# Optimization experiments

Hardware: AMD Instinct MI355X
Metric: run time of the kernel (lower is better)

## Reference

```python
import jax, jax.numpy as jnp
import numpy as np

# Model dims (from ModelArgs defaults)
B, S, DIM = 1, 1024, 2880
H, HKV, HD = 64, 8, 64        # query heads, kv heads, head dim
GROUP = H // HKV              # 8 query heads per kv head
WINDOW = 128                  # sliding window (layer_idx=0 -> active)
THETA = 150000.0


def setup_inputs() -> dict:
    key = jax.random.key(0)
    ks = jax.random.split(key, 10)
    rn = lambda k, shape, sc: (jax.random.normal(k, shape, jnp.float32) * sc)
    return {
        "x": rn(ks[0], (B, S, DIM), 1.0),
        "wq_w": rn(ks[1], (H * HD, DIM), 0.02),
        "wq_b": rn(ks[2], (H * HD,), 0.02),
        "wk_w": rn(ks[3], (HKV * HD, DIM), 0.02),
        "wk_b": rn(ks[4], (HKV * HD,), 0.02),
        "wv_w": rn(ks[5], (HKV * HD, DIM), 0.02),
        "wv_b": rn(ks[6], (HKV * HD,), 0.02),
        "wo_w": rn(ks[7], (DIM, H * HD), 0.02),
        "wo_b": rn(ks[8], (DIM,), 0.02),
        "sinks": rn(ks[9], (H,), 1.0),
    }


def _rope(t):
    # t: [B, S, h, HD]; half-split (rotate_half) RoPE with base THETA
    half = HD // 2
    inv_freq = 1.0 / (THETA ** (jnp.arange(half, dtype=jnp.float32) * 2.0 / HD))
    ang = jnp.arange(S, dtype=jnp.float32)[:, None] * inv_freq      # [S, half]
    cos = jnp.cos(ang)[None, :, None, :]
    sin = jnp.sin(ang)[None, :, None, :]
    t1, t2 = t[..., :half], t[..., half:]
    return jnp.concatenate([t1 * cos - t2 * sin, t1 * sin + t2 * cos], axis=-1)


def reference(x, wq_w, wq_b, wk_w, wk_b, wv_w, wv_b, wo_w, wo_b, sinks):
    # Projections (nn.Linear: y = x @ W^T + b)
    q = (jnp.einsum('bsd,ed->bse', x, wq_w) + wq_b).reshape(B, S, H, HD)
    k = (jnp.einsum('bsd,ed->bse', x, wk_w) + wk_b).reshape(B, S, HKV, HD)
    v = (jnp.einsum('bsd,ed->bse', x, wv_w) + wv_b).reshape(B, S, HKV, HD)

    q = _rope(q)
    k = _rope(k)

    # GQA: expand kv heads to match query heads
    k = jnp.repeat(k, GROUP, axis=2)   # [B, S, H, HD]
    v = jnp.repeat(v, GROUP, axis=2)

    scale = HD ** -0.5
    scores = jnp.einsum('bihd,bjhd->bhij', q, k) * scale   # [B, H, S, S]

    # Causal + sliding-window mask: attend to j with 0 <= i-j < WINDOW
    i = jnp.arange(S)[:, None]
    j = jnp.arange(S)[None, :]
    allowed = (j <= i) & ((i - j) < WINDOW)
    scores = jnp.where(allowed, scores, jnp.float32(-1e30))

    # Softmax with per-head learnable sink logit folded into normalization
    sink = sinks[None, :, None, None]                       # [1, H, 1, 1]
    m = jnp.maximum(jnp.max(scores, axis=-1, keepdims=True), sink)
    e = jnp.exp(scores - m)
    denom = jnp.sum(e, axis=-1, keepdims=True) + jnp.exp(sink - m)
    probs = e / denom                                       # sink mass dropped

    out = jnp.einsum('bhij,bjhd->bihd', probs, v).reshape(B, S, H * HD)
    return jnp.einsum('bse,de->bsd', out, wo_w) + wo_b
```

## Files before the change

kernel.cpp:

```cpp
#include <hip/hip_runtime.h>

typedef __attribute__((ext_vector_type(4))) float f32x4;
typedef __attribute__((ext_vector_type(8))) short s16x8;
typedef unsigned short u16;

#define DEVI __device__ __forceinline__

DEVI u16 f2bf(float f) {
    union { float f; unsigned int u; } v; v.f = f;
    unsigned int r = v.u + 0x7FFFu + ((v.u >> 16) & 1u);
    return (u16)(r >> 16);
}
DEVI float bf2f(u16 b) {
    union { unsigned int u; float f; } v; v.u = ((unsigned int)b) << 16;
    return v.f;
}

typedef __attribute__((address_space(1))) void gv_t;
typedef __attribute__((address_space(3))) void sv_t;

#define GLOAD16(SRC, DST) __builtin_amdgcn_global_load_lds( \
    (gv_t*)(SRC), (sv_t*)(DST), 16, 0, 0)

DEVI f32x4 mfma_bf16(s16x8 a, s16x8 b, f32x4 c) {
    return __builtin_amdgcn_mfma_f32_16x16x32_bf16(a, b, c, 0, 0, 0);
}

__global__ void cvt1_kernel(
    const float* __restrict__ x,  const float* __restrict__ wq, const float* __restrict__ wk,
    const float* __restrict__ wv,
    u16* __restrict__ xb, u16* __restrict__ wqb, u16* __restrict__ wkb,
    u16* __restrict__ wvb)
{
    int id = blockIdx.x * 256 + threadIdx.x;
    const float* s; u16* d; int off;
    if      (id < 737280)  { s = x;  d = xb;  off = id; }
    else if (id < 3686400) { s = wq; d = wqb; off = id - 737280; }
    else if (id < 4055040) { s = wk; d = wkb; off = id - 3686400; }
    else                   { s = wv; d = wvb; off = id - 4055040; }
    f32x4 v = *(const f32x4*)(s + (size_t)off * 4);
    union { u16 u[4]; unsigned long long ll; } o;
    #pragma unroll
    for (int j = 0; j < 4; ++j) o.u[j] = f2bf(v[j]);
    *(unsigned long long*)(d + (size_t)off * 4) = o.ll;
}

__global__ void cvt_wo_kernel(const float* __restrict__ wo, u16* __restrict__ wob)
{
    int id = blockIdx.x * 256 + threadIdx.x;
    f32x4 v = *(const f32x4*)(wo + (size_t)id * 4);
    union { u16 u[4]; unsigned long long ll; } o;
    #pragma unroll
    for (int j = 0; j < 4; ++j) o.u[j] = f2bf(v[j]);
    *(unsigned long long*)(wob + (size_t)id * 4) = o.ll;
}

__global__ __launch_bounds__(256, 2) void gemm_bf16nt(
    const u16* __restrict__ A, int lda, int kit, int ntot,
    const u16* __restrict__ W0, int t0, int n0, int c0,
    const u16* __restrict__ W1, int t1, int n1, int c1,
    const u16* __restrict__ W2, int t2, int n2, int c2,
    u16* __restrict__ C, int ldc, long long cstride)
{
    __shared__ u16 Als[2][128 * 64];
    __shared__ u16 Bls[2][128 * 64];

    const int lin = blockIdx.x;
    const int xc  = lin & 7;
    const int mm  = lin >> 3;
    const int nbl = xc + 8 * (mm >> 3);
    const int yt  = mm & 7;
    if (nbl >= ntot) return;

    const int tid  = threadIdx.x;
    const int lane = tid & 63;
    const int wid  = tid >> 6;
    const int li   = lane & 15;
    const int lg   = lane >> 4;
    const int m0   = yt * 128;

    const u16* W; int nt0, nsz, cb;
    if (nbl < t0)           { W = W0; nt0 = nbl * 128;             nsz = n0; cb = c0; }
    else if (nbl < t0 + t1) { W = W1; nt0 = (nbl - t0) * 128;      nsz = n1; cb = c1; }
    else                    { W = W2; nt0 = (nbl - t0 - t1) * 128; nsz = n2; cb = c2; }

    const int z  = blockIdx.z;
    const int S  = gridDim.z;
    const int it0 = (z * kit) / S;
    const int it1 = ((z + 1) * kit) / S;
    u16* Cp = C + (long long)z * cstride;

    const int wm = (wid >> 1) * 64;
    const int wn = (wid & 1) * 64;

    f32x4 acc[4][4];
    #pragma unroll
    for (int mi = 0; mi < 4; ++mi)
        #pragma unroll
        for (int ni = 0; ni < 4; ++ni)
            acc[mi][ni] = (f32x4){0.f, 0.f, 0.f, 0.f};

    const int srow = tid >> 3;
    const int slc  = (tid & 7) ^ (srow & 7);

#define STAGE(BUF, IT)                                                          \
    do {                                                                        \
        int k0_ = (IT) * 64;                                                    \
        _Pragma("unroll")                                                       \
        for (int s_ = 0; s_ < 4; ++s_) {                                        \
            const u16* sa_ = A + (size_t)(m0 + s_ * 32 + srow) * lda + k0_ + slc * 8; \
            GLOAD16(sa_, &Als[BUF][(s_ * 256 + wid * 64) * 8]);                 \
        }                                                                       \
        _Pragma("unroll")                                                       \
        for (int s_ = 0; s_ < 4; ++s_) {                                        \
            int wr_ = nt0 + s_ * 32 + srow;                                     \
            if (wr_ > nsz - 1) wr_ = nsz - 1;                                   \
            const u16* sb_ = W + (size_t)wr_ * lda + k0_ + slc * 8;             \
            GLOAD16(sb_, &Bls[BUF][(s_ * 256 + wid * 64) * 8]);                 \
        }                                                                       \
    } while (0)

    STAGE(0, it0);
    asm volatile("" ::: "memory");
    STAGE(1, it0 + 1);

    for (int it = it0; it < it1; ++it) {
        const int cur = (it - it0) & 1;

        if (it + 1 < it1) {
            asm volatile("s_waitcnt vmcnt(8)\n\ts_barrier" ::: "memory");
        } else {
            asm volatile("s_waitcnt vmcnt(0)\n\ts_barrier" ::: "memory");
        }

        s16x8 af[4][2], bfv[4][2];
        #pragma unroll
        for (int mi = 0; mi < 4; ++mi)
            #pragma unroll
            for (int kc = 0; kc < 2; ++kc) {
                int row = wm + mi * 16 + li;
                int ch  = (kc * 4 + lg) ^ (row & 7);
                af[mi][kc] = *(const s16x8*)&Als[cur][row * 64 + ch * 8];
            }
        #pragma unroll
        for (int ni = 0; ni < 4; ++ni)
            #pragma unroll
            for (int kc = 0; kc < 2; ++kc) {
                int row = wn + ni * 16 + li;
                int ch  = (kc * 4 + lg) ^ (row & 7);
                bfv[ni][kc] = *(const s16x8*)&Bls[cur][row * 64 + ch * 8];
            }
        #pragma unroll
        for (int mi = 0; mi < 4; ++mi)
            #pragma unroll
            for (int ni = 0; ni < 4; ++ni)
                #pragma unroll
                for (int kc = 0; kc < 2; ++kc)
                    acc[mi][ni] = mfma_bf16(af[mi][kc], bfv[ni][kc], acc[mi][ni]);

        asm volatile("s_waitcnt lgkmcnt(0)\n\ts_barrier" ::: "memory");

        if (it + 2 < it1) STAGE(cur, it + 2);
    }
#undef STAGE

    #pragma unroll
    for (int ni = 0; ni < 4; ++ni) {
        int colr = nt0 + wn + ni * 16 + li;
        if (colr < nsz) {
            #pragma unroll
            for (int mi = 0; mi < 4; ++mi)
                #pragma unroll
                for (int r = 0; r < 4; ++r) {
                    int row = m0 + wm + mi * 16 + lg * 4 + r;
                    Cp[(size_t)row * ldc + cb + colr] = f2bf(acc[mi][ni][r]);
                }
        }
    }
}

__global__ void rope_kernel(const u16* __restrict__ qkvp,
                            const float* __restrict__ qb, const float* __restrict__ kb,
                            const float* __restrict__ vb,
                            u16* __restrict__ qo, u16* __restrict__ ko, u16* __restrict__ vo)
{
    const long long PST = 1024LL * 5120;
    int id = blockIdx.x * 256 + threadIdx.x;
    int s  = id / 2560;
    int r  = id % 2560;
    const u16* r0 = qkvp + (size_t)s * 5120;
    if (r < 2304) {
        bool isq = r < 2048;
        int rr   = isq ? r : r - 2048;
        int hh   = rr >> 5;
        int d    = rr & 31;
        int col  = (isq ? 0 : 4096) + hh * 64 + d;
        int bcol = isq ? col : col - 4096;
        const float* bias = isq ? qb : kb;
        float t1 = bf2f(r0[col])      + bf2f(r0[col + PST])      + bf2f(r0[col + 2 * PST])      + bias[bcol];
        float t2 = bf2f(r0[col + 32]) + bf2f(r0[col + 32 + PST]) + bf2f(r0[col + 32 + 2 * PST]) + bias[bcol + 32];
        float ang = (float)s * exp2f((float)d * -0.5373314f);
        float sn, cs;
        sincosf(ang, &sn, &cs);
        float sc = isq ? 0.125f : 1.0f;
        float o1 = (t1 * cs - t2 * sn) * sc;
        float o2 = (t1 * sn + t2 * cs) * sc;
        u16* dst = isq ? qo : ko;
        int ldd  = isq ? 4096 : 512;
        dst[(size_t)s * ldd + bcol]      = f2bf(o1);
        dst[(size_t)s * ldd + bcol + 32] = f2bf(o2);
    } else {
        int e = (r - 2304) * 2;
        int c0 = 4608 + e;
        float v0 = bf2f(r0[c0])     + bf2f(r0[c0 + PST])     + bf2f(r0[c0 + 2 * PST])     + vb[e];
        float v1 = bf2f(r0[c0 + 1]) + bf2f(r0[c0 + 1 + PST]) + bf2f(r0[c0 + 1 + 2 * PST]) + vb[e + 1];
        vo[(size_t)s * 512 + e]     = f2bf(v0);
        vo[(size_t)s * 512 + e + 1] = f2bf(v1);
    }
}

__global__ void reduce_out_kernel(const u16* __restrict__ parts,
                                  const float* __restrict__ bias,
                                  float* __restrict__ out)
{
    int id = blockIdx.x * 256 + threadIdx.x;
    const long long stride = 1024LL * 2880;
    long long base = (long long)id * 8;
    float s[8];
    #pragma unroll
    for (int j = 0; j < 8; ++j) s[j] = 0.f;
    #pragma unroll
    for (int p = 0; p < 5; ++p) {
        s16x8 v = *(const s16x8*)(parts + p * stride + base);
        #pragma unroll
        for (int j = 0; j < 8; ++j) s[j] += bf2f((u16)v[j]);
    }
    int cb = (int)(base % 2880);
    f32x4 b0 = *(const f32x4*)(bias + cb);
    f32x4 b1 = *(const f32x4*)(bias + cb + 4);
    f32x4 o0 = {s[0] + b0[0], s[1] + b0[1], s[2] + b0[2], s[3] + b0[3]};
    f32x4 o1 = {s[4] + b1[0], s[5] + b1[1], s[6] + b1[2], s[7] + b1[3]};
    *(f32x4*)(out + base)     = o0;
    *(f32x4*)(out + base + 4) = o1;
}

__global__ __launch_bounds__(256, 2) void attn_kernel(
    const u16* __restrict__ Q, const u16* __restrict__ Kb, const u16* __restrict__ Vb,
    const float* __restrict__ sinks, u16* __restrict__ Ob)
{
    __shared__ u16 Kls[64 * 64];
    __shared__ u16 Pls[4][16 * 72];

    const int h    = blockIdx.x;
    const int qblk = blockIdx.y;
    const int kvh  = h >> 3;
    const int tid  = threadIdx.x;
    const int lane = tid & 63;
    const int w    = tid >> 6;
    const int li   = lane & 15;
    const int lg   = lane >> 4;
    const int qw   = qblk * 64 + w * 16;

    s16x8 aq[2];
    {
        const u16* qrow = Q + ((size_t)(qw + li) * 64 + h) * 64 + lg * 8;
        aq[0] = *(const s16x8*)(qrow);
        aq[1] = *(const s16x8*)(qrow + 32);
    }

    const float snk = sinks[h];
    float m_run[4], l_run[4];
    f32x4 oacc[4];
    #pragma unroll
    for (int r = 0; r < 4; ++r) { m_run[r] = snk; l_run[r] = 1.0f; }
    #pragma unroll
    for (int ni = 0; ni < 4; ++ni) oacc[ni] = (f32x4){0.f, 0.f, 0.f, 0.f};

    const int srow = tid >> 3;
    const int slc  = (tid & 7) ^ (srow & 7);

    for (int t = 0; t < 3; ++t) {
        int jt = qblk - 2 + t;
        if (jt < 0) continue;
        int j0 = jt * 64;

        #pragma unroll
        for (int it = 0; it < 2; ++it) {
            const u16* src = Kb + ((size_t)(j0 + it * 32 + srow) * 8 + kvh) * 64 + slc * 8;
            GLOAD16(src, &Kls[(it * 256 + w * 64) * 8]);
        }
        __syncthreads();

        f32x4 sc[4];
        #pragma unroll
        for (int nf = 0; nf < 4; ++nf) {
            sc[nf] = (f32x4){0.f, 0.f, 0.f, 0.f};
            #pragma unroll
            for (int kc = 0; kc < 2; ++kc) {
                int row = nf * 16 + li;
                int ch  = (kc * 4 + lg) ^ (row & 7);
                s16x8 bk = *(const s16x8*)&Kls[row * 64 + ch * 8];
                sc[nf] = mfma_bf16(aq[kc], bk, sc[nf]);
            }
        }

        #pragma unroll
        for (int r = 0; r < 4; ++r) {
            const int qg = qw + lg * 4 + r;
            float mx = -1e30f;
            #pragma unroll
            for (int nf = 0; nf < 4; ++nf) {
                int jg = j0 + nf * 16 + li;
                bool ok = (jg <= qg) && (qg - jg < 128);
                float v = ok ? sc[nf][r] : -1e30f;
                sc[nf][r] = v;
                mx = fmaxf(mx, v);
            }
            #pragma unroll
            for (int off = 1; off < 16; off <<= 1)
                mx = fmaxf(mx, __shfl_xor(mx, off));
            float mnew = fmaxf(m_run[r], mx);
            float corr = __expf(m_run[r] - mnew);
            m_run[r] = mnew;
            float rs = 0.f;
            #pragma unroll
            for (int nf = 0; nf < 4; ++nf) {
                float p = __expf(sc[nf][r] - mnew);
                rs += p;
                Pls[w][(lg * 4 + r) * 72 + nf * 16 + li] = f2bf(p);
            }
            #pragma unroll
            for (int off = 1; off < 16; off <<= 1)
                rs += __shfl_xor(rs, off);
            l_run[r] = l_run[r] * corr + rs;
            #pragma unroll
            for (int ni = 0; ni < 4; ++ni) oacc[ni][r] *= corr;
        }
        __syncthreads();

        #pragma unroll
        for (int kc = 0; kc < 2; ++kc) {
            s16x8 pa = *(const s16x8*)&Pls[w][li * 72 + kc * 32 + lg * 8];
            #pragma unroll
            for (int ni = 0; ni < 4; ++ni) {
                const u16* vsrc = Vb + ((size_t)(j0 + kc * 32 + lg * 8) * 8 + kvh) * 64 + ni * 16 + li;
                s16x8 bv;
                #pragma unroll
                for (int i = 0; i < 8; ++i) bv[i] = (short)vsrc[(size_t)i * 512];
                oacc[ni] = mfma_bf16(pa, bv, oacc[ni]);
            }
        }
    }

    #pragma unroll
    for (int r = 0; r < 4; ++r) {
        float inv = 1.0f / l_run[r];
        #pragma unroll
        for (int ni = 0; ni < 4; ++ni)
            Ob[((size_t)(qw + lg * 4 + r) * 64 + h) * 64 + ni * 16 + li] = f2bf(oacc[ni][r] * inv);
    }
}

extern "C" void kernel_launch(void* const* d_in, const int* in_sizes, int n_in,
                              void* d_out, int out_size, void* d_ws, size_t ws_size,
                              hipStream_t stream)
{
    const float* x     = (const float*)d_in[0];
    const float* wq_w  = (const float*)d_in[1];
    const float* wq_b  = (const float*)d_in[2];
    const float* wk_w  = (const float*)d_in[3];
    const float* wk_b  = (const float*)d_in[4];
    const float* wv_w  = (const float*)d_in[5];
    const float* wv_b  = (const float*)d_in[6];
    const float* wo_w  = (const float*)d_in[7];
    const float* wo_b  = (const float*)d_in[8];
    const float* sinks = (const float*)d_in[9];

    char* ws = (char*)d_ws;
    u16*   xb   = (u16*)(ws + 0);
    u16*   wqb  = (u16*)(ws + 5898240ULL);
    u16*   wkb  = (u16*)(ws + 29491200ULL);
    u16*   wvb  = (u16*)(ws + 32440320ULL);
    u16*   qkvp = (u16*)(ws + 35389440ULL);
    u16*   qr   = (u16*)(ws + 0);
    u16*   kr   = (u16*)(ws + 8388608ULL);
    u16*   vbf  = (u16*)(ws + 9437184ULL);
    u16*   attb = (u16*)(ws + 10485760ULL);
    u16*   wob  = (u16*)(ws + 35389440ULL);
    u16*   oprt = (u16*)(ws + 58982400ULL);

    (void)in_sizes; (void)n_in; (void)out_size; (void)ws_size;

    cvt1_kernel<<<17280, 256, 0, stream>>>(x, wq_w, wk_w, wv_w, xb, wqb, wkb, wvb);
    gemm_bf16nt<<<dim3(320, 1, 3), 256, 0, stream>>>(xb, 2880, 45, 40,
        wqb, 32, 4096, 0,
        wkb, 4, 512, 4096,
        wvb, 4, 512, 4608,
        qkvp, 5120, 1024LL * 5120);
    rope_kernel<<<10240, 256, 0, stream>>>(qkvp, wq_b, wk_b, wv_b, qr, kr, vbf);
    cvt_wo_kernel<<<11520, 256, 0, stream>>>(wo_w, wob);
    attn_kernel<<<dim3(64, 16), 256, 0, stream>>>(qr, kr, vbf, sinks, attb);
    gemm_bf16nt<<<dim3(192, 1, 5), 256, 0, stream>>>(attb, 4096, 64, 23,
        wob, 23, 2880, 0,
        wob, 0, 0, 0,
        wob, 0, 0, 0,
        oprt, 2880, 1024LL * 2880);
    reduce_out_kernel<<<1440, 256, 0, stream>>>(oprt, wo_b, (float*)d_out);
}
```

Before: 140.1 us.

## Single-buffer GEMM with higher occupancy, vectorize RoPE, merge weight conversions

The GEMM drops its double-buffered LDS prefetch and uses a single stage with __syncthreads, raising launch bounds to 3 blocks per SM so that occupancy, rather than software pipelining, hides load latency. The RoPE/bias kernel now processes 8 elements per thread with 16-byte vector loads and stores. The wo conversion is folded into the main conversion kernel, and wob moves to its own workspace region, removing one launch. The risk is that the GEMM loses load/compute overlap within each block.

After: 130.9 us. 1.07x faster.

```diff
diff --git a/kernel.cpp b/kernel.cpp
--- a/kernel.cpp
+++ b/kernel.cpp
@@ -26,18 +26,19 @@
     return __builtin_amdgcn_mfma_f32_16x16x32_bf16(a, b, c, 0, 0, 0);
 }
 
-__global__ void cvt1_kernel(
+__global__ void cvt_all_kernel(
     const float* __restrict__ x,  const float* __restrict__ wq, const float* __restrict__ wk,
-    const float* __restrict__ wv,
+    const float* __restrict__ wv, const float* __restrict__ wo,
     u16* __restrict__ xb, u16* __restrict__ wqb, u16* __restrict__ wkb,
-    u16* __restrict__ wvb)
+    u16* __restrict__ wvb, u16* __restrict__ wob)
 {
     int id = blockIdx.x * 256 + threadIdx.x;
     const float* s; u16* d; int off;
     if      (id < 737280)  { s = x;  d = xb;  off = id; }
     else if (id < 3686400) { s = wq; d = wqb; off = id - 737280; }
     else if (id < 4055040) { s = wk; d = wkb; off = id - 3686400; }
-    else                   { s = wv; d = wvb; off = id - 4055040; }
+    else if (id < 4423680) { s = wv; d = wvb; off = id - 4055040; }
+    else                   { s = wo; d = wob; off = id - 4423680; }
     f32x4 v = *(const f32x4*)(s + (size_t)off * 4);
     union { u16 u[4]; unsigned long long ll; } o;
     #pragma unroll
@@ -45,25 +46,15 @@
     *(unsigned long long*)(d + (size_t)off * 4) = o.ll;
 }
 
-__global__ void cvt_wo_kernel(const float* __restrict__ wo, u16* __restrict__ wob)
-{
-    int id = blockIdx.x * 256 + threadIdx.x;
-    f32x4 v = *(const f32x4*)(wo + (size_t)id * 4);
-    union { u16 u[4]; unsigned long long ll; } o;
-    #pragma unroll
-    for (int j = 0; j < 4; ++j) o.u[j] = f2bf(v[j]);
-    *(unsigned long long*)(wob + (size_t)id * 4) = o.ll;
-}
-
-__global__ __launch_bounds__(256, 2) void gemm_bf16nt(
+__global__ __launch_bounds__(256, 3) void gemm_m97(
     const u16* __restrict__ A, int lda, int kit, int ntot,
     const u16* __restrict__ W0, int t0, int n0, int c0,
     const u16* __restrict__ W1, int t1, int n1, int c1,
     const u16* __restrict__ W2, int t2, int n2, int c2,
     u16* __restrict__ C, int ldc, long long cstride)
 {
-    __shared__ u16 Als[2][128 * 64];
-    __shared__ u16 Bls[2][128 * 64];
+    __shared__ u16 Als[128 * 64];
+    __shared__ u16 Bls[128 * 64];
 
     const int lin = blockIdx.x;
     const int xc  = lin & 7;
@@ -103,35 +94,21 @@
     const int srow = tid >> 3;
     const int slc  = (tid & 7) ^ (srow & 7);
 
-#define STAGE(BUF, IT)                                                          \
-    do {                                                                        \
-        int k0_ = (IT) * 64;                                                    \
-        _Pragma("unroll")                                                       \
-        for (int s_ = 0; s_ < 4; ++s_) {                                        \
-            const u16* sa_ = A + (size_t)(m0 + s_ * 32 + srow) * lda + k0_ + slc * 8; \
-            GLOAD16(sa_, &Als[BUF][(s_ * 256 + wid * 64) * 8]);                 \
-        }                                                                       \
-        _Pragma("unroll")                                                       \
-        for (int s_ = 0; s_ < 4; ++s_) {                                        \
-            int wr_ = nt0 + s_ * 32 + srow;                                     \
-            if (wr_ > nsz - 1) wr_ = nsz - 1;                                   \
-            const u16* sb_ = W + (size_t)wr_ * lda + k0_ + slc * 8;             \
-            GLOAD16(sb_, &Bls[BUF][(s_ * 256 + wid * 64) * 8]);                 \
-        }                                                                       \
-    } while (0)
-
-    STAGE(0, it0);
-    asm volatile("" ::: "memory");
-    STAGE(1, it0 + 1);
-
     for (int it = it0; it < it1; ++it) {
-        const int cur = (it - it0) & 1;
-
-        if (it + 1 < it1) {
-            asm volatile("s_waitcnt vmcnt(8)\n\ts_barrier" ::: "memory");
-        } else {
-            asm volatile("s_waitcnt vmcnt(0)\n\ts_barrier" ::: "memory");
-        }
+        const int k0 = it * 64;
+        #pragma unroll
+        for (int s_ = 0; s_ < 4; ++s_) {
+            const u16* sa = A + (size_t)(m0 + s_ * 32 + srow) * lda + k0 + slc * 8;
+            GLOAD16(sa, &Als[(s_ * 256 + tid) * 8]);
+        }
+        #pragma unroll
+        for (int s_ = 0; s_ < 4; ++s_) {
+            int wr = nt0 + s_ * 32 + srow;
+            if (wr > nsz - 1) wr = nsz - 1;
+            const u16* sb = W + (size_t)wr * lda + k0 + slc * 8;
+            GLOAD16(sb, &Bls[(s_ * 256 + tid) * 8]);
+        }
+        __syncthreads();
 
         s16x8 af[4][2], bfv[4][2];
         #pragma unroll
@@ -140,7 +117,7 @@
             for (int kc = 0; kc < 2; ++kc) {
                 int row = wm + mi * 16 + li;
                 int ch  = (kc * 4 + lg) ^ (row & 7);
-                af[mi][kc] = *(const s16x8*)&Als[cur][row * 64 + ch * 8];
+                af[mi][kc] = *(const s16x8*)&Als[row * 64 + ch * 8];
             }
         #pragma unroll
         for (int ni = 0; ni < 4; ++ni)
@@ -148,7 +125,7 @@
             for (int kc = 0; kc < 2; ++kc) {
                 int row = wn + ni * 16 + li;
                 int ch  = (kc * 4 + lg) ^ (row & 7);
-                bfv[ni][kc] = *(const s16x8*)&Bls[cur][row * 64 + ch * 8];
+                bfv[ni][kc] = *(const s16x8*)&Bls[row * 64 + ch * 8];
             }
         #pragma unroll
         for (int mi = 0; mi < 4; ++mi)
@@ -157,12 +134,8 @@
                 #pragma unroll
                 for (int kc = 0; kc < 2; ++kc)
                     acc[mi][ni] = mfma_bf16(af[mi][kc], bfv[ni][kc], acc[mi][ni]);
-
-        asm volatile("s_waitcnt lgkmcnt(0)\n\ts_barrier" ::: "memory");
-
-        if (it + 2 < it1) STAGE(cur, it + 2);
-    }
-#undef STAGE
+        __syncthreads();
+    }
 
     #pragma unroll
     for (int ni = 0; ni < 4; ++ni) {
@@ -186,36 +159,63 @@
 {
     const long long PST = 1024LL * 5120;
     int id = blockIdx.x * 256 + threadIdx.x;
-    int s  = id / 2560;
-    int r  = id % 2560;
+    int s  = id / 352;
+    int g  = id % 352;
     const u16* r0 = qkvp + (size_t)s * 5120;
-    if (r < 2304) {
-        bool isq = r < 2048;
-        int rr   = isq ? r : r - 2048;
-        int hh   = rr >> 5;
-        int d    = rr & 31;
-        int col  = (isq ? 0 : 4096) + hh * 64 + d;
-        int bcol = isq ? col : col - 4096;
+
+    if (g < 288) {
+        bool isq = g < 256;
+        int gg   = isq ? g : g - 256;
+        int hh   = gg >> 2;
+        int dg   = gg & 3;
+        int col0 = (isq ? 0 : 4096) + hh * 64 + dg * 8;
+        int bcol = isq ? col0 : col0 - 4096;
         const float* bias = isq ? qb : kb;
-        float t1 = bf2f(r0[col])      + bf2f(r0[col + PST])      + bf2f(r0[col + 2 * PST])      + bias[bcol];
-        float t2 = bf2f(r0[col + 32]) + bf2f(r0[col + 32 + PST]) + bf2f(r0[col + 32 + 2 * PST]) + bias[bcol + 32];
-        float ang = (float)s * exp2f((float)d * -0.5373314f);
-        float sn, cs;
-        sincosf(ang, &sn, &cs);
+
+        float t1[8], t2[8];
+        #pragma unroll
+        for (int e = 0; e < 8; ++e) { t1[e] = bias[bcol + e]; t2[e] = bias[bcol + 32 + e]; }
+        #pragma unroll
+        for (int p = 0; p < 3; ++p) {
+            s16x8 lo = *(const s16x8*)(r0 + col0 + p * PST);
+            s16x8 hi = *(const s16x8*)(r0 + col0 + 32 + p * PST);
+            #pragma unroll
+            for (int e = 0; e < 8; ++e) {
+                t1[e] += bf2f((u16)lo[e]);
+                t2[e] += bf2f((u16)hi[e]);
+            }
+        }
         float sc = isq ? 0.125f : 1.0f;
-        float o1 = (t1 * cs - t2 * sn) * sc;
-        float o2 = (t1 * sn + t2 * cs) * sc;
+        s16x8 o1, o2;
+        #pragma unroll
+        for (int e = 0; e < 8; ++e) {
+            int d = dg * 8 + e;
+            float ang = (float)s * exp2f((float)d * -0.5373314f);
+            float sn, cs;
+            sincosf(ang, &sn, &cs);
+            o1[e] = (short)f2bf((t1[e] * cs - t2[e] * sn) * sc);
+            o2[e] = (short)f2bf((t1[e] * sn + t2[e] * cs) * sc);
+        }
         u16* dst = isq ? qo : ko;
         int ldd  = isq ? 4096 : 512;
-        dst[(size_t)s * ldd + bcol]      = f2bf(o1);
-        dst[(size_t)s * ldd + bcol + 32] = f2bf(o2);
+        *(s16x8*)(dst + (size_t)s * ldd + bcol)      = o1;
+        *(s16x8*)(dst + (size_t)s * ldd + bcol + 32) = o2;
     } else {
-        int e = (r - 2304) * 2;
-        int c0 = 4608 + e;
-        float v0 = bf2f(r0[c0])     + bf2f(r0[c0 + PST])     + bf2f(r0[c0 + 2 * PST])     + vb[e];
-        float v1 = bf2f(r0[c0 + 1]) + bf2f(r0[c0 + 1 + PST]) + bf2f(r0[c0 + 1 + 2 * PST]) + vb[e + 1];
-        vo[(size_t)s * 512 + e]     = f2bf(v0);
-        vo[(size_t)s * 512 + e + 1] = f2bf(v1);
+        int gg   = g - 288;
+        int col0 = 4608 + gg * 8;
+        float t[8];
+        #pragma unroll
+        for (int e = 0; e < 8; ++e) t[e] = vb[gg * 8 + e];
+        #pragma unroll
+        for (int p = 0; p < 3; ++p) {
+            s16x8 v = *(const s16x8*)(r0 + col0 + p * PST);
+            #pragma unroll
+            for (int e = 0; e < 8; ++e) t[e] += bf2f((u16)v[e]);
+        }
+        s16x8 o;
+        #pragma unroll
+        for (int e = 0; e < 8; ++e) o[e] = (short)f2bf(t[e]);
+        *(s16x8*)(vo + (size_t)s * 512 + gg * 8) = o;
     }
 }
 
@@ -386,21 +386,21 @@
     u16*   kr   = (u16*)(ws + 8388608ULL);
     u16*   vbf  = (u16*)(ws + 9437184ULL);
     u16*   attb = (u16*)(ws + 10485760ULL);
-    u16*   wob  = (u16*)(ws + 35389440ULL);
     u16*   oprt = (u16*)(ws + 58982400ULL);
+    u16*   wob  = (u16*)(ws + 88473600ULL);
 
     (void)in_sizes; (void)n_in; (void)out_size; (void)ws_size;
 
-    cvt1_kernel<<<17280, 256, 0, stream>>>(x, wq_w, wk_w, wv_w, xb, wqb, wkb, wvb);
-    gemm_bf16nt<<<dim3(320, 1, 3), 256, 0, stream>>>(xb, 2880, 45, 40,
+    cvt_all_kernel<<<28800, 256, 0, stream>>>(x, wq_w, wk_w, wv_w, wo_w,
+                                              xb, wqb, wkb, wvb, wob);
+    gemm_m97<<<dim3(320, 1, 3), 256, 0, stream>>>(xb, 2880, 45, 40,
         wqb, 32, 4096, 0,
         wkb, 4, 512, 4096,
         wvb, 4, 512, 4608,
         qkvp, 5120, 1024LL * 5120);
-    rope_kernel<<<10240, 256, 0, stream>>>(qkvp, wq_b, wk_b, wv_b, qr, kr, vbf);
-    cvt_wo_kernel<<<11520, 256, 0, stream>>>(wo_w, wob);
+    rope_kernel<<<1408, 256, 0, stream>>>(qkvp, wq_b, wk_b, wv_b, qr, kr, vbf);
     attn_kernel<<<dim3(64, 16), 256, 0, stream>>>(qr, kr, vbf, sinks, attb);
-    gemm_bf16nt<<<dim3(192, 1, 5), 256, 0, stream>>>(attb, 4096, 64, 23,
+    gemm_m97<<<dim3(192, 1, 5), 256, 0, stream>>>(attb, 4096, 64, 23,
         wob, 23, 2880, 0,
         wob, 0, 0, 0,
         wob, 0, 0, 0,
```
